# Performance work log

Hardware: AMD Instinct MI355X
Metric: run time of the kernel (lower is better)

## Reference

```python
import jax, jax.numpy as jnp
import numpy as np

EMB = 1024

def setup_inputs() -> dict:
    key = jax.random.key(0)
    ks = jax.random.split(key, 10)
    B, S, E = 8, 2048, EMB
    x = jax.random.normal(ks[0], (B, S, E), dtype=jnp.float32)
    context = jax.random.normal(ks[1], (B, S, E), dtype=jnp.float32)
    pad_mask = jax.random.randint(ks[2], (B, S, S), 0, 2) == 1
    s = 1.0 / np.sqrt(E)
    Wq = jax.random.normal(ks[3], (E, E), dtype=jnp.float32) * s
    bq = jnp.zeros((E,), dtype=jnp.float32)
    Wk = jax.random.normal(ks[4], (E, E), dtype=jnp.float32) * s
    bk = jnp.zeros((E,), dtype=jnp.float32)
    Wv = jax.random.normal(ks[5], (E, E), dtype=jnp.float32) * s
    bv = jnp.zeros((E,), dtype=jnp.float32)
    return {"x": x, "context": context, "pad_mask": pad_mask,
            "Wq": Wq, "bq": bq, "Wk": Wk, "bk": bk, "Wv": Wv, "bv": bv}

def reference(x, context, pad_mask, Wq, bq, Wk, bk, Wv, bv):
    scale = x.shape[-1] ** (-0.5)
    Q = jnp.einsum('bse,fe->bsf', x, Wq) + bq
    K = jnp.einsum('bse,fe->bsf', context, Wk) + bk
    V = jnp.einsum('bse,fe->bsf', context, Wv) + bv
    att = jnp.einsum('bid,bjd->bij', Q, K) * scale
    att = jnp.where(pad_mask, jnp.float32(-1e9), att)
    att = jax.nn.softmax(att, axis=-1)
    out = jnp.einsum('bij,bjk->bik', att, V)
    return (out, att)
```

## Files before the change

kernel.cpp:

```cpp
#include <hip/hip_runtime.h>
#include <hip/hip_bf16.h>
#include <type_traits>

typedef __attribute__((ext_vector_type(8))) __bf16 bf16x8;
typedef __attribute__((ext_vector_type(4))) float f32x4;
typedef unsigned short u16;

__device__ __forceinline__ u16 f2b(float x) {
  union { __hip_bfloat16 b; u16 u; } cv;
  cv.b = __float2bfloat16(x);
  return cv.u;
}

__device__ __forceinline__ void ld16(const u16* g, u16* l) {
  __builtin_amdgcn_global_load_lds(
      (const __attribute__((address_space(1))) unsigned int*)g,
      (__attribute__((address_space(3))) unsigned int*)l, 16, 0, 0);
}

constexpr int BM = 256, BN = 256, BK = 64;

enum { EPI_NONE = 0, EPI_BIAS = 1, EPI_BIAS_T = 2, EPI_MASK = 3 };

#define PHASE(QR, QC, LA, LB, BUF)                                            \
  {                                                                           \
    if (LA) {                                                                 \
      _Pragma("unroll") for (int i = 0; i < 4; ++i)                           \
          _Pragma("unroll") for (int ks = 0; ks < 2; ++ks)                    \
              aF[i][ks] = *(const bf16x8*)&As[BUF][                           \
                  (wr * 128 + QR * 64 + i * 16 + fr) * BK +                   \
                  (((ks * 4 + quad) ^ (fr & 7)) * 8)];                        \
    }                                                                         \
    if (LB) {                                                                 \
      _Pragma("unroll") for (int j = 0; j < 2; ++j)                           \
          _Pragma("unroll") for (int ks = 0; ks < 2; ++ks)                    \
              bF[j][ks] = *(const bf16x8*)&Bs[BUF][                           \
                  (wc * 64 + QC * 32 + j * 16 + fr) * BK +                    \
                  (((ks * 4 + quad) ^ (fr & 7)) * 8)];                        \
    }                                                                         \
    __builtin_amdgcn_s_barrier();                                             \
    __builtin_amdgcn_s_setprio(1);                                            \
    _Pragma("unroll") for (int i = 0; i < 4; ++i)                             \
        _Pragma("unroll") for (int j = 0; j < 2; ++j)                         \
            _Pragma("unroll") for (int ks = 0; ks < 2; ++ks)                  \
                acc[QR * 4 + i][QC * 2 + j] =                                 \
                    __builtin_amdgcn_mfma_f32_16x16x32_bf16(                  \
                        aF[i][ks], bF[j][ks], acc[QR * 4 + i][QC * 2 + j],    \
                        0, 0, 0);                                             \
    __builtin_amdgcn_s_setprio(0);                                            \
    __builtin_amdgcn_s_barrier();                                             \
  }

template <typename TC, int EPI>
__global__ __launch_bounds__(512, 2) void gemm_bt(
    const u16* __restrict__ A, const u16* __restrict__ Bt, TC* __restrict__ C,
    const float* __restrict__ bias, const int* __restrict__ mask, float scale,
    int N, int K, long long sA, long long sB, long long sC, long long sM) {
  __shared__ u16 As[2][BM * BK];
  __shared__ u16 Bs[2][BN * BK];

  const int bz = blockIdx.z;
  A += (size_t)bz * sA;
  Bt += (size_t)bz * sB;
  C += (size_t)bz * sC;
  const long long maskBase = (long long)bz * sM;

  const int m0 = blockIdx.y * BM, n0 = blockIdx.x * BN;
  const int t = threadIdx.x, wave = t >> 6, lane = t & 63;
  const int wr = wave >> 2, wc = wave & 3;
  const int fr = lane & 15, quad = lane >> 4;
  const int lr = lane >> 3, lc = lane & 7;

  const u16* ga = A + (size_t)(m0 + wave * 8 + lr) * K + (lc ^ lr) * 8;
  const u16* gb = Bt + (size_t)(n0 + wave * 8 + lr) * K + (lc ^ lr) * 8;

  f32x4 acc[8][4] = {};
  bf16x8 aF[4][2], bF[2][2];

  const int nt = K / BK;

  auto STAGE = [&](int kt, int bsel) {
    const size_t ko = (size_t)kt * BK;
#pragma unroll
    for (int i = 0; i < 4; ++i) {
      ld16(ga + (size_t)(i * 64) * K + ko,
           &As[bsel][(i * 64 + wave * 8) * BK]);
      ld16(gb + (size_t)(i * 64) * K + ko,
           &Bs[bsel][(i * 64 + wave * 8) * BK]);
    }
  };

  STAGE(0, 0);
  STAGE(1, 1);

  for (int kt = 0; kt < nt; ++kt) {
    const int b = kt & 1;
    if (kt + 1 < nt)
      __builtin_amdgcn_s_waitcnt(0x0f78);
    else
      __builtin_amdgcn_s_waitcnt(0x0f70);
    __builtin_amdgcn_s_barrier();
    __builtin_amdgcn_sched_barrier(0);

    PHASE(0, 0, 1, 1, b)
    PHASE(0, 1, 0, 1, b)
    PHASE(1, 1, 1, 0, b)
    PHASE(1, 0, 0, 1, b)

    __builtin_amdgcn_sched_barrier(0);
    if (kt + 2 < nt) STAGE(kt + 2, b);
  }

#pragma unroll
  for (int i = 0; i < 8; ++i)
#pragma unroll
    for (int j = 0; j < 4; ++j) {
      const int mb = m0 + wr * 128 + i * 16 + quad * 4;
      const int n = n0 + wc * 64 + j * 16 + fr;
      if constexpr (EPI == EPI_BIAS_T) {
        const float bb = bias[n];
        const int b = mb >> 11, ml = mb & 2047;
        ushort4 o;
        o.x = f2b(acc[i][j][0] + bb);
        o.y = f2b(acc[i][j][1] + bb);
        o.z = f2b(acc[i][j][2] + bb);
        o.w = f2b(acc[i][j][3] + bb);
        *(ushort4*)&((u16*)C)[(size_t)b * 2097152 + (size_t)n * 2048 + ml] = o;
      } else {
#pragma unroll
        for (int r = 0; r < 4; ++r) {
          const int m = mb + r;
          float v = acc[i][j][r];
          if constexpr (EPI == EPI_BIAS) v += bias[n];
          if constexpr (EPI == EPI_MASK)
            v = mask[maskBase + (size_t)m * N + n] ? -1e9f : v * scale;
          if constexpr (std::is_same_v<TC, u16>)
            C[(size_t)m * N + n] = f2b(v);
          else
            C[(size_t)m * N + n] = v;
        }
      }
    }
}

__global__ __launch_bounds__(256) void cast_all(
    const float* __restrict__ x, const float* __restrict__ ctx,
    const float* __restrict__ wq, const float* __restrict__ wk,
    const float* __restrict__ wv, u16* __restrict__ xb, u16* __restrict__ cb,
    u16* __restrict__ wqb, u16* __restrict__ wkb, u16* __restrict__ wvb) {
  int b = blockIdx.x;
  const float* s;
  u16* d;
  size_t off;
  if (b < 16384) { s = x; d = xb; off = b; }
  else if (b < 32768) { s = ctx; d = cb; off = b - 32768 + 16384; }
  else if (b < 33792) { s = wq; d = wqb; off = b - 32768; }
  else if (b < 34816) { s = wk; d = wkb; off = b - 33792; }
  else { s = wv; d = wvb; off = b - 34816; }
  const size_t i = (off * 256 + threadIdx.x) * 4;
  float4 v = *(const float4*)&s[i];
  ushort4 h;
  h.x = f2b(v.x); h.y = f2b(v.y); h.z = f2b(v.z); h.w = f2b(v.w);
  *(ushort4*)&d[i] = h;
}

__device__ __forceinline__ float blockReduceMax(float v, float* red) {
#pragma unroll
  for (int o = 32; o > 0; o >>= 1) v = fmaxf(v, __shfl_down(v, o));
  int t = threadIdx.x;
  if ((t & 63) == 0) red[t >> 6] = v;
  __syncthreads();
  float r = fmaxf(fmaxf(red[0], red[1]), fmaxf(red[2], red[3]));
  __syncthreads();
  return r;
}

__device__ __forceinline__ float blockReduceSum(float v, float* red) {
#pragma unroll
  for (int o = 32; o > 0; o >>= 1) v += __shfl_down(v, o);
  int t = threadIdx.x;
  if ((t & 63) == 0) red[t >> 6] = v;
  __syncthreads();
  float r = red[0] + red[1] + red[2] + red[3];
  __syncthreads();
  return r;
}

__global__ __launch_bounds__(256) void softmax_rows(float* __restrict__ att,
                                                    u16* __restrict__ attb) {
  __shared__ float red[4];
  float* p = att + (size_t)blockIdx.x * 2048;
  u16* pb = attb + (size_t)blockIdx.x * 2048;
  const int t = threadIdx.x;
  float4 v0 = ((const float4*)p)[t];
  float4 v1 = ((const float4*)p)[t + 256];
  float mx = fmaxf(fmaxf(fmaxf(v0.x, v0.y), fmaxf(v0.z, v0.w)),
                   fmaxf(fmaxf(v1.x, v1.y), fmaxf(v1.z, v1.w)));
  mx = blockReduceMax(mx, red);
  float4 e0, e1;
  e0.x = __expf(v0.x - mx); e0.y = __expf(v0.y - mx);
  e0.z = __expf(v0.z - mx); e0.w = __expf(v0.w - mx);
  e1.x = __expf(v1.x - mx); e1.y = __expf(v1.y - mx);
  e1.z = __expf(v1.z - mx); e1.w = __expf(v1.w - mx);
  float s = (e0.x + e0.y + e0.z + e0.w) + (e1.x + e1.y + e1.z + e1.w);
  s = blockReduceSum(s, red);
  float inv = 1.0f / s;
  e0.x *= inv; e0.y *= inv; e0.z *= inv; e0.w *= inv;
  e1.x *= inv; e1.y *= inv; e1.z *= inv; e1.w *= inv;
  ((float4*)p)[t] = e0;
  ((float4*)p)[t + 256] = e1;
  ushort4 h0, h1;
  h0.x = f2b(e0.x); h0.y = f2b(e0.y); h0.z = f2b(e0.z); h0.w = f2b(e0.w);
  h1.x = f2b(e1.x); h1.y = f2b(e1.y); h1.z = f2b(e1.z); h1.w = f2b(e1.w);
  *(ushort4*)&pb[(size_t)t * 4] = h0;
  *(ushort4*)&pb[(size_t)(t + 256) * 4] = h1;
}

extern "C" void kernel_launch(void* const* d_in, const int* in_sizes, int n_in,
                              void* d_out, int out_size, void* d_ws,
                              size_t ws_size, hipStream_t stream) {
  const float* x   = (const float*)d_in[0];
  const float* ctx = (const float*)d_in[1];
  const int*   msk = (const int*)d_in[2];
  const float* Wq  = (const float*)d_in[3];
  const float* bq  = (const float*)d_in[4];
  const float* Wk  = (const float*)d_in[5];
  const float* bk  = (const float*)d_in[6];
  const float* Wv  = (const float*)d_in[7];
  const float* bv  = (const float*)d_in[8];

  float* out = (float*)d_out;
  float* att = out + 16777216;

  u16* xb = (u16*)d_ws;
  u16* cb = xb + 16777216;
  u16* Q  = cb + 16777216;
  u16* Kb = Q + 16777216;
  u16* Vt = xb;
  u16* attb = Q;
  u16* wqb = (u16*)att;
  u16* wkb = wqb + 1048576;
  u16* wvb = wkb + 1048576;

  dim3 blk(256), blkg(512);
  const long long SQ = 2048LL * 1024, SS = 2048LL * 2048, SV = 1024LL * 2048;

  cast_all<<<dim3(35840), blk, 0, stream>>>(x, ctx, Wq, Wk, Wv, xb, cb, wqb,
                                            wkb, wvb);

  gemm_bt<u16, EPI_BIAS><<<dim3(4, 64, 1), blkg, 0, stream>>>(
      xb, wqb, Q, bq, nullptr, 0.f, 1024, 1024, 0, 0, 0, 0);
  gemm_bt<u16, EPI_BIAS><<<dim3(4, 64, 1), blkg, 0, stream>>>(
      cb, wkb, Kb, bk, nullptr, 0.f, 1024, 1024, 0, 0, 0, 0);
  gemm_bt<u16, EPI_BIAS_T><<<dim3(4, 64, 1), blkg, 0, stream>>>(
      cb, wvb, Vt, bv, nullptr, 0.f, 1024, 1024, 0, 0, 0, 0);

  gemm_bt<float, EPI_MASK><<<dim3(8, 8, 8), blkg, 0, stream>>>(
      Q, Kb, att, nullptr, msk, 0.03125f, 2048, 1024, SQ, SQ, SS, SS);

  softmax_rows<<<dim3(16384), blk, 0, stream>>>(att, attb);

  gemm_bt<float, EPI_NONE><<<dim3(4, 8, 8), blkg, 0, stream>>>(
      attb, Vt, out, nullptr, nullptr, 0.f, 1024, 2048, SS, SV, SQ, 0);
}
```

Before: 749.4 us.

## Move mask/scale into softmax and drop per-phase barriers in GEMM

The QK^T GEMM epilogue no longer reads the pad mask or applies the scale. Softmax now loads the mask with vectorized int4 reads and applies mask and scale before the max reduction. In the GEMM main loop, the two barriers and setprio around each of the four MFMA phases are removed, leaving a single barrier after the phases and before staging the next tile. This cuts synchronisation overhead and makes mask reads coalesced, but gives up the wave-priority interleaving that the phased schedule relied on.

```diff
diff --git a/kernel.cpp b/kernel.cpp
--- a/kernel.cpp
+++ b/kernel.cpp
@@ -20,7 +20,7 @@
 
 constexpr int BM = 256, BN = 256, BK = 64;
 
-enum { EPI_NONE = 0, EPI_BIAS = 1, EPI_BIAS_T = 2, EPI_MASK = 3 };
+enum { EPI_NONE = 0, EPI_BIAS = 1, EPI_BIAS_T = 2 };
 
 #define PHASE(QR, QC, LA, LB, BUF)                                            \
   {                                                                           \
@@ -38,8 +38,6 @@
                   (wc * 64 + QC * 32 + j * 16 + fr) * BK +                    \
                   (((ks * 4 + quad) ^ (fr & 7)) * 8)];                        \
     }                                                                         \
-    __builtin_amdgcn_s_barrier();                                             \
-    __builtin_amdgcn_s_setprio(1);                                            \
     _Pragma("unroll") for (int i = 0; i < 4; ++i)                             \
         _Pragma("unroll") for (int j = 0; j < 2; ++j)                         \
             _Pragma("unroll") for (int ks = 0; ks < 2; ++ks)                  \
@@ -47,15 +45,13 @@
                     __builtin_amdgcn_mfma_f32_16x16x32_bf16(                  \
                         aF[i][ks], bF[j][ks], acc[QR * 4 + i][QC * 2 + j],    \
                         0, 0, 0);                                             \
-    __builtin_amdgcn_s_setprio(0);                                            \
-    __builtin_amdgcn_s_barrier();                                             \
   }
 
 template <typename TC, int EPI>
 __global__ __launch_bounds__(512, 2) void gemm_bt(
     const u16* __restrict__ A, const u16* __restrict__ Bt, TC* __restrict__ C,
-    const float* __restrict__ bias, const int* __restrict__ mask, float scale,
-    int N, int K, long long sA, long long sB, long long sC, long long sM) {
+    const float* __restrict__ bias, float scale, int N, int K, long long sA,
+    long long sB, long long sC) {
   __shared__ u16 As[2][BM * BK];
   __shared__ u16 Bs[2][BN * BK];
 
@@ -63,7 +59,6 @@
   A += (size_t)bz * sA;
   Bt += (size_t)bz * sB;
   C += (size_t)bz * sC;
-  const long long maskBase = (long long)bz * sM;
 
   const int m0 = blockIdx.y * BM, n0 = blockIdx.x * BN;
   const int t = threadIdx.x, wave = t >> 6, lane = t & 63;
@@ -108,6 +103,7 @@
     PHASE(1, 0, 0, 1, b)
 
     __builtin_amdgcn_sched_barrier(0);
+    __builtin_amdgcn_s_barrier();
     if (kt + 2 < nt) STAGE(kt + 2, b);
   }
 
@@ -132,8 +128,6 @@
           const int m = mb + r;
           float v = acc[i][j][r];
           if constexpr (EPI == EPI_BIAS) v += bias[n];
-          if constexpr (EPI == EPI_MASK)
-            v = mask[maskBase + (size_t)m * N + n] ? -1e9f : v * scale;
           if constexpr (std::is_same_v<TC, u16>)
             C[(size_t)m * N + n] = f2b(v);
           else
@@ -187,13 +181,26 @@
 }
 
 __global__ __launch_bounds__(256) void softmax_rows(float* __restrict__ att,
-                                                    u16* __restrict__ attb) {
+                                                    u16* __restrict__ attb,
+                                                    const int* __restrict__ msk,
+                                                    float scale) {
   __shared__ float red[4];
   float* p = att + (size_t)blockIdx.x * 2048;
+  const int* mr = msk + (size_t)blockIdx.x * 2048;
   u16* pb = attb + (size_t)blockIdx.x * 2048;
   const int t = threadIdx.x;
   float4 v0 = ((const float4*)p)[t];
   float4 v1 = ((const float4*)p)[t + 256];
+  int4 q0 = ((const int4*)mr)[t];
+  int4 q1 = ((const int4*)mr)[t + 256];
+  v0.x = q0.x ? -1e9f : v0.x * scale;
+  v0.y = q0.y ? -1e9f : v0.y * scale;
+  v0.z = q0.z ? -1e9f : v0.z * scale;
+  v0.w = q0.w ? -1e9f : v0.w * scale;
+  v1.x = q1.x ? -1e9f : v1.x * scale;
+  v1.y = q1.y ? -1e9f : v1.y * scale;
+  v1.z = q1.z ? -1e9f : v1.z * scale;
+  v1.w = q1.w ? -1e9f : v1.w * scale;
   float mx = fmaxf(fmaxf(fmaxf(v0.x, v0.y), fmaxf(v0.z, v0.w)),
                    fmaxf(fmaxf(v1.x, v1.y), fmaxf(v1.z, v1.w)));
   mx = blockReduceMax(mx, red);
@@ -249,17 +256,17 @@
                                             wkb, wvb);
 
   gemm_bt<u16, EPI_BIAS><<<dim3(4, 64, 1), blkg, 0, stream>>>(
-      xb, wqb, Q, bq, nullptr, 0.f, 1024, 1024, 0, 0, 0, 0);
+      xb, wqb, Q, bq, 0.f, 1024, 1024, 0, 0, 0);
   gemm_bt<u16, EPI_BIAS><<<dim3(4, 64, 1), blkg, 0, stream>>>(
-      cb, wkb, Kb, bk, nullptr, 0.f, 1024, 1024, 0, 0, 0, 0);
+      cb, wkb, Kb, bk, 0.f, 1024, 1024, 0, 0, 0);
   gemm_bt<u16, EPI_BIAS_T><<<dim3(4, 64, 1), blkg, 0, stream>>>(
-      cb, wvb, Vt, bv, nullptr, 0.f, 1024, 1024, 0, 0, 0, 0);
-
-  gemm_bt<float, EPI_MASK><<<dim3(8, 8, 8), blkg, 0, stream>>>(
-      Q, Kb, att, nullptr, msk, 0.03125f, 2048, 1024, SQ, SQ, SS, SS);
-
-  softmax_rows<<<dim3(16384), blk, 0, stream>>>(att, attb);
+      cb, wvb, Vt, bv, 0.f, 1024, 1024, 0, 0, 0);
+
+  gemm_bt<float, EPI_NONE><<<dim3(8, 8, 8), blkg, 0, stream>>>(
+      Q, Kb, att, nullptr, 0.f, 2048, 1024, SQ, SQ, SS);
+
+  softmax_rows<<<dim3(16384), blk, 0, stream>>>(att, attb, msk, 0.03125f);
 
   gemm_bt<float, EPI_NONE><<<dim3(4, 8, 8), blkg, 0, stream>>>(
-      attb, Vt, out, nullptr, nullptr, 0.f, 1024, 2048, SS, SV, SQ, 0);
-}
+      attb, Vt, out, nullptr, 0.f, 1024, 2048, SS, SV, SQ);
+}
```

Result: faster. 696.9 us (-7.0%).
